# Optimization experiments

Hardware: AMD Instinct MI355X
Metric: run time of the kernel (lower is better)

## Reference

```python
import jax, jax.numpy as jnp
import numpy as np
import math

HIDDEN, N_HEADS = 128, 4
HEAD_DIM = HIDDEN // N_HEADS

def _silu(x):
    return x * jax.nn.sigmoid(x)

def _ln(x, g, b, eps=1e-5):
    m = jnp.mean(x, axis=-1, keepdims=True)
    v = jnp.mean((x - m) ** 2, axis=-1, keepdims=True)
    return (x - m) / jnp.sqrt(v + eps) * g + b


def setup_inputs() -> dict:
    key = jax.random.key(0)
    B, N, ND, ED, HD = 2, 512, 64, 32, 128
    ks = iter(jax.random.split(key, 64))
    def p(*shape):
        return jax.random.normal(next(ks), shape, jnp.float32) * 0.05
    d = {}
    d['h'] = jax.random.normal(next(ks), (B, N, ND), jnp.float32)
    d['x'] = jax.random.normal(next(ks), (B, N, 2), jnp.float32)
    d['e'] = jax.random.normal(next(ks), (B, N, N, ED), jnp.float32)
    msg_in = 2 * ND + ED + 1  # 161
    d['msg_W1'] = p(msg_in, HD); d['msg_b1'] = jnp.zeros((HD,), jnp.float32)
    d['msg_ln_g'] = jnp.ones((HD,), jnp.float32); d['msg_ln_b'] = jnp.zeros((HD,), jnp.float32)
    d['msg_W2'] = p(HD, HD); d['msg_b2'] = jnp.zeros((HD,), jnp.float32)
    d['msg_W3'] = p(HD, HD); d['msg_b3'] = jnp.zeros((HD,), jnp.float32)
    d['attn_W1'] = p(HD, HD // 2); d['attn_b1'] = jnp.zeros((HD // 2,), jnp.float32)
    d['attn_W2'] = p(HD // 2, N_HEADS); d['attn_b2'] = jnp.zeros((N_HEADS,), jnp.float32)
    d['val_W'] = p(HD, HD); d['val_b'] = jnp.zeros((HD,), jnp.float32)
    d['coord_W1'] = p(HD, HD // 2); d['coord_b1'] = jnp.zeros((HD // 2,), jnp.float32)
    d['coord_W2'] = p(HD // 2, 1)  # bias=False
    d['node_W1'] = p(ND + HD, HD); d['node_b1'] = jnp.zeros((HD,), jnp.float32)
    d['node_ln_g'] = jnp.ones((HD,), jnp.float32); d['node_ln_b'] = jnp.zeros((HD,), jnp.float32)
    d['node_W2'] = p(HD, ND); d['node_b2'] = jnp.zeros((ND,), jnp.float32)
    d['edge_W1'] = p(ED + HD, HD); d['edge_b1'] = jnp.zeros((HD,), jnp.float32)
    d['edge_ln_g'] = jnp.ones((HD,), jnp.float32); d['edge_ln_b'] = jnp.zeros((HD,), jnp.float32)
    d['edge_W2'] = p(HD, ED); d['edge_b2'] = jnp.zeros((ED,), jnp.float32)
    d['nn_g'] = jnp.ones((ND,), jnp.float32); d['nn_b'] = jnp.zeros((ND,), jnp.float32)
    d['en_g'] = jnp.ones((ED,), jnp.float32); d['en_b'] = jnp.zeros((ED,), jnp.float32)
    d['coord_scale'] = jnp.float32(0.1)
    return d


def reference(h, x, e,
              msg_W1, msg_b1, msg_ln_g, msg_ln_b, msg_W2, msg_b2, msg_W3, msg_b3,
              attn_W1, attn_b1, attn_W2, attn_b2, val_W, val_b,
              coord_W1, coord_b1, coord_W2,
              node_W1, node_b1, node_ln_g, node_ln_b, node_W2, node_b2,
              edge_W1, edge_b1, edge_ln_g, edge_ln_b, edge_W2, edge_b2,
              nn_g, nn_b, en_g, en_b, coord_scale):
    B, N, ND = h.shape
    # pairwise geometry: x_diff[b,i,j] = x[b,j] - x[b,i]
    x_diff = x[:, None, :, :] - x[:, :, None, :]           # (B,N,N,2)
    distances = jnp.linalg.norm(x_diff, axis=-1, keepdims=True)  # (B,N,N,1)
    h_i = jnp.broadcast_to(h[:, :, None, :], (B, N, N, ND))
    h_j = jnp.broadcast_to(h[:, None, :, :], (B, N, N, ND))
    msg_input = jnp.concatenate([h_i, h_j, e, distances], axis=-1)
    # message MLP (dropout is identity in eval)
    m = _silu(msg_input @ msg_W1 + msg_b1)
    m = _ln(m, msg_ln_g, msg_ln_b)
    m = _silu(m @ msg_W2 + msg_b2)
    messages = m @ msg_W3 + msg_b3                          # (B,N,N,HIDDEN)
    # attention over j (axis=2), multi-head
    attn_logits = (_silu(messages @ attn_W1 + attn_b1) @ attn_W2 + attn_b2)
    attn_logits = attn_logits / math.sqrt(HEAD_DIM)
    attn_weights = jax.nn.softmax(attn_logits, axis=2)      # (B,N,N,H)
    values = (messages @ val_W + val_b).reshape(B, N, N, N_HEADS, HEAD_DIM)
    messages_attended = jnp.einsum('bijh,bijhd->bihd', attn_weights, values)
    messages_attended = messages_attended.reshape(B, N, HIDDEN)
    # equivariant coordinate update
    coord_weights = _silu(messages @ coord_W1 + coord_b1) @ coord_W2  # (B,N,N,1)
    coord_weights = jnp.tanh(coord_weights / 10.0)
    x_diff_norm = x_diff / (distances + 1e-8)
    coord_update = jnp.sum(coord_weights * x_diff_norm, axis=2)      # (B,N,2)
    x_new = x + coord_scale * coord_update
    # node update
    h_input = jnp.concatenate([h, messages_attended], axis=-1)
    hh = _silu(h_input @ node_W1 + node_b1)
    hh = _ln(hh, node_ln_g, node_ln_b)
    hh = hh @ node_W2 + node_b2
    h_new = _ln(h + hh, nn_g, nn_b)
    # edge update
    e_input = jnp.concatenate([e, messages], axis=-1)
    ee = _silu(e_input @ edge_W1 + edge_b1)
    ee = _ln(ee, edge_ln_g, edge_ln_b)
    ee = ee @ edge_W2 + edge_b2
    e_new = _ln(e + ee, en_g, en_b)
    return (h_new, x_new, e_new)
```

## Files before the change

kernel.cpp:

```cpp
#include <hip/hip_runtime.h>
#include <math.h>

typedef __attribute__((ext_vector_type(8))) short short8;
typedef __attribute__((ext_vector_type(4))) short short4v;
typedef __attribute__((ext_vector_type(8))) unsigned short u16x8;
typedef __attribute__((ext_vector_type(4))) float f32x4;

#define NN 512
#define JT 32
#define STR 136
#define BUFSZ (JT * STR)
#define E2S 36

#define TOT_W 106496

__device__ __forceinline__ unsigned short f2b(float x) {
    unsigned int u = __float_as_uint(x);
    unsigned int r = (u + 0x7FFFu + ((u >> 16) & 1u)) >> 16;
    return (unsigned short)r;
}
__device__ __forceinline__ float b2f(unsigned short v) {
    return __uint_as_float(((unsigned int)v) << 16);
}
__device__ __forceinline__ float silu_f(float v) { return v / (1.f + __expf(-v)); }

__device__ __forceinline__ float half_sum(float v, float* s_red, int t) {
    s_red[t] = v;
    __syncthreads();
    int tt = t & 127;
    for (int s = 64; s > 0; s >>= 1) {
        if (tt < s) s_red[t] += s_red[t + s];
        __syncthreads();
    }
    float r = s_red[t & 128];
    __syncthreads();
    return r;
}

__device__ __forceinline__ void frag_kf(int loc, int nK, int& k, int& f) {
    int jj = loc & 7;
    int lane = (loc >> 3) & 63;
    int fs = loc >> 9;
    int ks = fs % nK;
    int ft = fs / nK;
    k = ks * 32 + ((lane >> 4) << 3) + jj;
    f = ft * 16 + (lane & 15);
}

extern "C" __global__ void prepack_w(const float* __restrict__ msg_W1, const float* __restrict__ msg_W2,
                                     const float* __restrict__ msg_W3, const float* __restrict__ val_W,
                                     const float* __restrict__ attn_W1, const float* __restrict__ coord_W1,
                                     const float* __restrict__ edge_W1, const float* __restrict__ edge_W2,
                                     unsigned short* __restrict__ ws) {
    int idx = blockIdx.x * 256 + threadIdx.x;
    if (idx >= TOT_W) return;
    float v;
    int k, f;
    if (idx < 16384) {
        frag_kf(idx, 4, k, f);
        v = (k <= 96) ? msg_W1[(64 + k) * 128 + f] : 0.f;
    } else if (idx < 32768) {
        frag_kf(idx - 16384, 4, k, f);
        v = msg_W2[k * 128 + f];
    } else if (idx < 49152) {
        frag_kf(idx - 32768, 4, k, f);
        v = msg_W3[k * 128 + f];
    } else if (idx < 65536) {
        frag_kf(idx - 49152, 4, k, f);
        v = val_W[k * 128 + f];
    } else if (idx < 81920) {
        frag_kf(idx - 65536, 4, k, f);
        v = (f < 64) ? attn_W1[k * 64 + f] : coord_W1[k * 64 + (f - 64)];
    } else if (idx < 102400) {
        frag_kf(idx - 81920, 5, k, f);
        v = (k < 128) ? edge_W1[(32 + k) * 128 + f] : edge_W1[(k - 128) * 128 + f];
    } else {
        frag_kf(idx - 102400, 4, k, f);
        v = edge_W2[k * 32 + f];
    }
    ws[idx] = f2b(v);
}

struct Frag2x2 { f32x4 a[2][2]; };

__device__ __forceinline__ short8 wfrag(const unsigned short* base, int nK, int ft, int ks, int lane) {
    return *(const short8*)(base + (((ft * nK + ks) << 9) + (lane << 3)));
}

__device__ __forceinline__ void initF(Frag2x2& F, const float* bias, int ftA, int lane) {
    int q = lane >> 4;
    f32x4 bA = *(const f32x4*)(bias + ftA * 16 + q * 4);
    f32x4 bB = *(const f32x4*)(bias + (ftA + 1) * 16 + q * 4);
    F.a[0][0] = bA; F.a[0][1] = bA;
    F.a[1][0] = bB; F.a[1][1] = bB;
}

__device__ __forceinline__ void ldb(const unsigned short* B, int kcol, int lane, short8& b0, short8& b1) {
    int q8 = ((lane >> 4) << 3), l15 = lane & 15;
    b0 = *(const short8*)(B + l15 * STR + kcol + q8);
    b1 = *(const short8*)(B + (16 + l15) * STR + kcol + q8);
}

__device__ __forceinline__ void mfma4(Frag2x2& F, short8 a0, short8 a1, short8 b0, short8 b1) {
    F.a[0][0] = __builtin_amdgcn_mfma_f32_16x16x32_bf16(a0, b0, F.a[0][0], 0, 0, 0);
    F.a[0][1] = __builtin_amdgcn_mfma_f32_16x16x32_bf16(a0, b1, F.a[0][1], 0, 0, 0);
    F.a[1][0] = __builtin_amdgcn_mfma_f32_16x16x32_bf16(a1, b0, F.a[1][0], 0, 0, 0);
    F.a[1][1] = __builtin_amdgcn_mfma_f32_16x16x32_bf16(a1, b1, F.a[1][1], 0, 0, 0);
}

__device__ __forceinline__ void storeF(const Frag2x2& F, unsigned short* dbuf, int ftA, int lane, int act) {
    int q = lane >> 4, l15 = lane & 15;
#pragma unroll
    for (int fi = 0; fi < 2; fi++)
#pragma unroll
        for (int ji = 0; ji < 2; ji++) {
            int j = ji * 16 + l15;
            int f0 = (ftA + fi) * 16 + q * 4;
            f32x4 v = F.a[fi][ji];
            short4v p;
#pragma unroll
            for (int r = 0; r < 4; r++) {
                float o = act ? silu_f(v[r]) : v[r];
                p[r] = (short)f2b(o);
            }
            *(short4v*)(dbuf + j * STR + f0) = p;
        }
}

__device__ __forceinline__ void ln_tile(unsigned short* buf, const float* g, const float* bv, int t) {
    int j = t >> 3, sub = t & 7;
    unsigned short* p = buf + j * STR + sub * 16;
    u16x8 r0 = *(u16x8*)p;
    u16x8 r1 = *(u16x8*)(p + 8);
    float v[16];
#pragma unroll
    for (int i = 0; i < 8; i++) { v[i] = b2f(r0[i]); v[8 + i] = b2f(r1[i]); }
    float sm = 0.f;
#pragma unroll
    for (int i = 0; i < 16; i++) sm += v[i];
    sm += __shfl_xor(sm, 1); sm += __shfl_xor(sm, 2); sm += __shfl_xor(sm, 4);
    float mean = sm * 0.0078125f;
    float sq = 0.f;
#pragma unroll
    for (int i = 0; i < 16; i++) { float d = v[i] - mean; sq += d * d; }
    sq += __shfl_xor(sq, 1); sq += __shfl_xor(sq, 2); sq += __shfl_xor(sq, 4);
    float rstd = rsqrtf(sq * 0.0078125f + 1e-5f);
    u16x8 o0, o1;
#pragma unroll
    for (int i = 0; i < 8; i++) {
        o0[i] = f2b((v[i] - mean) * rstd * g[sub * 16 + i] + bv[sub * 16 + i]);
        o1[i] = f2b((v[8 + i] - mean) * rstd * g[sub * 16 + 8 + i] + bv[sub * 16 + 8 + i]);
    }
    *(u16x8*)p = o0;
    *(u16x8*)(p + 8) = o1;
}

extern "C" __global__ __launch_bounds__(256, 2)
void egnn_mfma(const float* __restrict__ h, const float* __restrict__ x, const float* __restrict__ e,
               const float* __restrict__ msg_W1, const float* __restrict__ msg_b1,
               const float* __restrict__ msg_ln_g, const float* __restrict__ msg_ln_b,
               const float* __restrict__ msg_b2, const float* __restrict__ msg_b3,
               const float* __restrict__ attn_b1, const float* __restrict__ attn_W2,
               const float* __restrict__ attn_b2, const float* __restrict__ val_b,
               const float* __restrict__ coord_b1, const float* __restrict__ coord_W2,
               const float* __restrict__ node_W1, const float* __restrict__ node_b1,
               const float* __restrict__ node_ln_g, const float* __restrict__ node_ln_b,
               const float* __restrict__ node_W2, const float* __restrict__ node_b2,
               const float* __restrict__ edge_b1, const float* __restrict__ edge_ln_g,
               const float* __restrict__ edge_ln_b, const float* __restrict__ edge_b2,
               const float* __restrict__ nn_g, const float* __restrict__ nn_b,
               const float* __restrict__ en_g, const float* __restrict__ en_b,
               const float* __restrict__ coord_scale_p,
               const unsigned short* __restrict__ wpk,
               float* __restrict__ out_h, float* __restrict__ out_x, float* __restrict__ out_e) {
    const int t = threadIdx.x;
    const int wave = t >> 6, lane = t & 63;
    const int biA = blockIdx.x * 2;
    const int biB = biA + 1;
    const int b = biA >> 9;

    __shared__ __align__(16) unsigned short smA[3 * BUFSZ];
    __shared__ __align__(16) unsigned short smB[3 * BUFSZ];
    unsigned short* B0a = smA;
    unsigned short* B1a = smA + BUFSZ;
    unsigned short* B2a = smA + 2 * BUFSZ;
    unsigned short* B0b = smB;
    unsigned short* B1b = smB + BUFSZ;
    unsigned short* B2b = smB + 2 * BUFSZ;
    __shared__ __align__(16) unsigned short s_e2a[32 * E2S];
    __shared__ __align__(16) unsigned short s_e2b[32 * E2S];

    __shared__ __align__(16) float s_bias1a[128], s_bias1b[128];
    __shared__ __align__(16) float s_b2c[128], s_b3c[128], s_bv[128], s_bac[128], s_be1[128];
    __shared__ __align__(16) float s_be2[32];
    __shared__ __align__(16) float s_mg[128], s_mb[128], s_eg[128], s_eb[128];
    __shared__ __align__(16) float s_cw2[64], s_aw2[4][64], s_ab2[4], s_eng[32], s_enb[32];
    __shared__ __align__(16) float s_lg[2][JT][4];
    __shared__ __align__(16) float s_hiA[64], s_hiB[64];

    const unsigned short* wG1 = wpk;
    const unsigned short* wG2 = wpk + 16384;
    const unsigned short* wG3 = wpk + 32768;
    const unsigned short* wV  = wpk + 49152;
    const unsigned short* wAC = wpk + 65536;
    const unsigned short* wE1 = wpk + 81920;
    const unsigned short* wE2 = wpk + 102400;

    if (t < 64) s_hiA[t] = h[(size_t)biA * 64 + t];
    else if (t < 128) s_hiB[t - 64] = h[(size_t)biB * 64 + (t - 64)];
    if (t < 128) {
        s_b2c[t] = msg_b2[t]; s_b3c[t] = msg_b3[t]; s_bv[t] = val_b[t];
        s_bac[t] = (t < 64) ? attn_b1[t] : coord_b1[t - 64];
        s_be1[t] = edge_b1[t];
        s_mg[t] = msg_ln_g[t]; s_mb[t] = msg_ln_b[t];
        s_eg[t] = edge_ln_g[t]; s_eb[t] = edge_ln_b[t];
    }
    if (t < 32) { s_be2[t] = edge_b2[t]; s_eng[t] = en_g[t]; s_enb[t] = en_b[t]; }
    if (t < 64) s_cw2[t] = coord_W2[t];
    { int hh = t >> 6, k = t & 63; s_aw2[hh][k] = attn_W2[k * 4 + hh]; }
    if (t < 4) s_ab2[t] = attn_b2[t];
    __syncthreads();
    {
        int ii = t >> 7, tt = t & 127;
        const float* hi = ii ? s_hiB : s_hiA;
        float acc = msg_b1[tt];
        for (int k = 0; k < 64; k++) acc = fmaf(hi[k], msg_W1[k * 128 + tt], acc);
        (ii ? s_bias1b : s_bias1a)[tt] = acc;
    }
    const float xiA0 = x[(size_t)biA * 2 + 0];
    const float xiA1 = x[(size_t)biA * 2 + 1];
    const float xiB0 = x[(size_t)biB * 2 + 0];
    const float xiB1 = x[(size_t)biB * 2 + 1];

    float m_run = -3e38f, l_run = 0.f, acc_run = 0.f;
    float cu_x = 0.f, cu_y = 0.f, xdn_x = 0.f, xdn_y = 0.f;

    const int q8 = ((lane >> 4) << 3), l15 = lane & 15;

#pragma unroll 1
    for (int j0 = 0; j0 < NN; j0 += JT) {
        {
            int j = t >> 3, sub = t & 7;
            int jj = j0 + j;
            const float* hp = h + ((size_t)(b * NN + jj)) * 64 + sub * 8;
            float4 h0 = *(const float4*)hp;
            float4 h1 = *(const float4*)(hp + 4);
            u16x8 o;
            o[0] = f2b(h0.x); o[1] = f2b(h0.y); o[2] = f2b(h0.z); o[3] = f2b(h0.w);
            o[4] = f2b(h1.x); o[5] = f2b(h1.y); o[6] = f2b(h1.z); o[7] = f2b(h1.w);
            *(u16x8*)(B0a + j * STR + sub * 8) = o;
            if (sub < 4) {
                const float* ea = e + ((size_t)biA * NN + jj) * 32 + sub * 8;
                float4 e0 = *(const float4*)ea;
                float4 e1 = *(const float4*)(ea + 4);
                u16x8 oe;
                oe[0] = f2b(e0.x); oe[1] = f2b(e0.y); oe[2] = f2b(e0.z); oe[3] = f2b(e0.w);
                oe[4] = f2b(e1.x); oe[5] = f2b(e1.y); oe[6] = f2b(e1.z); oe[7] = f2b(e1.w);
                *(u16x8*)(B0a + j * STR + 64 + sub * 8) = oe;
                const float* eb = e + ((size_t)biB * NN + jj) * 32 + sub * 8;
                float4 f0v = *(const float4*)eb;
                float4 f1v = *(const float4*)(eb + 4);
                u16x8 ob;
                ob[0] = f2b(f0v.x); ob[1] = f2b(f0v.y); ob[2] = f2b(f0v.z); ob[3] = f2b(f0v.w);
                ob[4] = f2b(f1v.x); ob[5] = f2b(f1v.y); ob[6] = f2b(f1v.z); ob[7] = f2b(f1v.w);
                *(u16x8*)(B0b + j * STR + 64 + sub * 8) = ob;
            } else if (sub > 4) {
                u16x8 z = (u16x8)0;
                *(u16x8*)(B0a + j * STR + 96 + (sub - 4) * 8) = z;
                *(u16x8*)(B0b + j * STR + 96 + (sub - 4) * 8) = z;
            }
        }
        if (t < JT) {
            int jj = j0 + t;
            float dx = x[(size_t)(b * NN + jj) * 2 + 0] - xiA0;
            float dy = x[(size_t)(b * NN + jj) * 2 + 1] - xiA1;
            float dist = sqrtf(dx * dx + dy * dy);
            float inv = 1.f / (dist + 1e-8f);
            xdn_x = dx * inv; xdn_y = dy * inv;
            u16x8 z = (u16x8)0;
            z[0] = f2b(dist);
            *(u16x8*)(B0a + t * STR + 96) = z;
        } else if (t >= 128 && t < 128 + JT) {
            int tb = t - 128;
            int jj = j0 + tb;
            float dx = x[(size_t)(b * NN + jj) * 2 + 0] - xiB0;
            float dy = x[(size_t)(b * NN + jj) * 2 + 1] - xiB1;
            float dist = sqrtf(dx * dx + dy * dy);
            float inv = 1.f / (dist + 1e-8f);
            xdn_x = dx * inv; xdn_y = dy * inv;
            u16x8 z = (u16x8)0;
            z[0] = f2b(dist);
            *(u16x8*)(B0b + tb * STR + 96) = z;
        }
        __syncthreads();

        {
            Frag2x2 Fa, Fb;
            initF(Fa, s_bias1a, wave * 2, lane);
            initF(Fb, s_bias1b, wave * 2, lane);
#pragma unroll
            for (int ks = 0; ks < 4; ks++) {
                short8 a0 = wfrag(wG1, 4, wave * 2, ks, lane);
                short8 a1 = wfrag(wG1, 4, wave * 2 + 1, ks, lane);
                short8 b0, b1;
                ldb(B0a, ks * 32, lane, b0, b1);
                mfma4(Fa, a0, a1, b0, b1);
                if (ks >= 2) ldb(B0b, ks * 32, lane, b0, b1);
                mfma4(Fb, a0, a1, b0, b1);
            }
            storeF(Fa, B1a, wave * 2, lane, 1);
            storeF(Fb, B1b, wave * 2, lane, 1);
        }
        __syncthreads();
        ln_tile(B1a, s_mg, s_mb, t);
        ln_tile(B1b, s_mg, s_mb, t);
        __syncthreads();

        {
            Frag2x2 Fa, Fb;
            initF(Fa, s_b2c, wave * 2, lane);
            initF(Fb, s_b2c, wave * 2, lane);
#pragma unroll
            for (int ks = 0; ks < 4; ks++) {
                short8 a0 = wfrag(wG2, 4, wave * 2, ks, lane);
                short8 a1 = wfrag(wG2, 4, wave * 2 + 1, ks, lane);
                short8 b0, b1;
                ldb(B1a, ks * 32, lane, b0, b1); mfma4(Fa, a0, a1, b0, b1);
                ldb(B1b, ks * 32, lane, b0, b1); mfma4(Fb, a0, a1, b0, b1);
            }
            storeF(Fa, B2a, wave * 2, lane, 1);
            storeF(Fb, B2b, wave * 2, lane, 1);
        }
        __syncthreads();

        {
            Frag2x2 Fa, Fb;
            initF(Fa, s_b3c, wave * 2, lane);
            initF(Fb, s_b3c, wave * 2, lane);
#pragma unroll
            for (int ks = 0; ks < 4; ks++) {
                short8 a0 = wfrag(wG3, 4, wave * 2, ks, lane);
                short8 a1 = wfrag(wG3, 4, wave * 2 + 1, ks, lane);
                short8 b0, b1;
                ldb(B2a, ks * 32, lane, b0, b1); mfma4(Fa, a0, a1, b0, b1);
                ldb(B2b, ks * 32, lane, b0, b1); mfma4(Fb, a0, a1, b0, b1);
            }
            storeF(Fa, B1a, wave * 2, lane, 0);
            storeF(Fb, B1b, wave * 2, lane, 0);
        }
        __syncthreads();

        {
            Frag2x2 FEa, FEb;
            initF(FEa, s_be1, wave * 2, lane);
            initF(FEb, s_be1, wave * 2, lane);
            {
                short8 a0 = wfrag(wE1, 5, wave * 2, 4, lane);
                short8 a1 = wfrag(wE1, 5, wave * 2 + 1, 4, lane);
                short8 b0, b1;
                ldb(B0a, 64, lane, b0, b1); mfma4(FEa, a0, a1, b0, b1);
                ldb(B0b, 64, lane, b0, b1); mfma4(FEb, a0, a1, b0, b1);
            }
            Frag2x2 FVa, FVb, FAa, FAb;
            initF(FVa, s_bv, wave * 2, lane);
            initF(FVb, s_bv, wave * 2, lane);
            initF(FAa, s_bac, wave * 2, lane);
            initF(FAb, s_bac, wave * 2, lane);
#pragma unroll
            for (int ks = 0; ks < 4; ks++) {
                short8 av0 = wfrag(wV, 4, wave * 2, ks, lane);
                short8 av1 = wfrag(wV, 4, wave * 2 + 1, ks, lane);
                short8 aa0 = wfrag(wAC, 4, wave * 2, ks, lane);
                short8 aa1 = wfrag(wAC, 4, wave * 2 + 1, ks, lane);
                short8 b0, b1;
                ldb(B1a, ks * 32, lane, b0, b1);
                mfma4(FVa, av0, av1, b0, b1);
                mfma4(FAa, aa0, aa1, b0, b1);
                ldb(B1b, ks * 32, lane, b0, b1);
                mfma4(FVb, av0, av1, b0, b1);
                mfma4(FAb, aa0, aa1, b0, b1);
            }
            storeF(FVa, B2a, wave * 2, lane, 0);
            storeF(FVb, B2b, wave * 2, lane, 0);
#pragma unroll
            for (int ks = 0; ks < 4; ks++) {
                short8 ae0 = wfrag(wE1, 5, wave * 2, ks, lane);
                short8 ae1 = wfrag(wE1, 5, wave * 2 + 1, ks, lane);
                short8 b0, b1;
                ldb(B1a, ks * 32, lane, b0, b1); mfma4(FEa, ae0, ae1, b0, b1);
                ldb(B1b, ks * 32, lane, b0, b1); mfma4(FEb, ae0, ae1, b0, b1);
            }
            __syncthreads();
            storeF(FAa, B0a, wave * 2, lane, 1);
            storeF(FAb, B0b, wave * 2, lane, 1);
            storeF(FEa, B1a, wave * 2, lane, 1);
            storeF(FEb, B1b, wave * 2, lane, 1);
        }
        __syncthreads();

        ln_tile(B1a, s_eg, s_eb, t);
        ln_tile(B1b, s_eg, s_eb, t);
        {
            int ii = t >> 7, tt = t & 127;
            const unsigned short* B0x = ii ? B0b : B0a;
            int j = tt >> 2, hh = tt & 3;
            float acc = s_ab2[hh];
#pragma unroll
            for (int m = 0; m < 8; m++) {
                u16x8 r = *(u16x8*)(B0x + j * STR + m * 8);
#pragma unroll
                for (int i = 0; i < 8; i++) acc = fmaf(b2f(r[i]), s_aw2[hh][m * 8 + i], acc);
            }
            s_lg[ii][j][hh] = acc * 0.17677669529663687f;
        }
        __syncthreads();

        {
            int ii = t >> 7, tt = t & 127;
            const unsigned short* B2x = ii ? B2b : B2a;
            int hh = tt >> 5;
#pragma unroll 4
            for (int j = 0; j < JT; j++) {
                float lg = s_lg[ii][j][hh];
                float nm = fmaxf(m_run, lg);
                float sc = __expf(m_run - nm);
                float p = __expf(lg - nm);
                float v = b2f(B2x[j * STR + tt]);
                acc_run = acc_run * sc + p * v;
                l_run = l_run * sc + p;
                m_run = nm;
            }
            if (tt < 32) {
                const unsigned short* B0x = ii ? B0b : B0a;
                float acc = 0.f;
#pragma unroll
                for (int m = 0; m < 8; m++) {
                    u16x8 r = *(u16x8*)(B0x + tt * STR + 64 + m * 8);
#pragma unroll
                    for (int i = 0; i < 8; i++) acc = fmaf(b2f(r[i]), s_cw2[m * 8 + i], acc);
                }
                float cw = tanhf(acc * 0.1f);
                cu_x = fmaf(cw, xdn_x, cu_x);
                cu_y = fmaf(cw, xdn_y, cu_y);
            }
        }
        __syncthreads();

        {
            int ih = wave >> 1, wv = wave & 1;
            const unsigned short* B1x = ih ? B1b : B1a;
            unsigned short* e2x = ih ? s_e2b : s_e2a;
            int q = lane >> 4;
            f32x4 bb = *(const f32x4*)(s_be2 + wv * 16 + q * 4);
            f32x4 a0 = bb, a1 = bb;
#pragma unroll
            for (int ks = 0; ks < 4; ks++) {
                short8 b0, b1;
                ldb(B1x, ks * 32, lane, b0, b1);
                short8 aw = wfrag(wE2, 4, wv, ks, lane);
                a0 = __builtin_amdgcn_mfma_f32_16x16x32_bf16(aw, b0, a0, 0, 0, 0);
                a1 = __builtin_amdgcn_mfma_f32_16x16x32_bf16(aw, b1, a1, 0, 0, 0);
            }
#pragma unroll
            for (int ji = 0; ji < 2; ji++) {
                int j = ji * 16 + l15;
                int f0 = wv * 16 + q * 4;
                f32x4 v = ji ? a1 : a0;
                short4v p;
#pragma unroll
                for (int r = 0; r < 4; r++) p[r] = (short)f2b(v[r]);
                *(short4v*)(e2x + j * E2S + f0) = p;
            }
        }
        __syncthreads();

#pragma unroll
        for (int ii = 0; ii < 2; ii++) {
            int biX = biA + ii;
            const unsigned short* e2x = ii ? s_e2b : s_e2a;
            int j = t >> 3, sub = t & 7;
            int jj = j0 + j;
            float4 ev = *(const float4*)(e + ((size_t)biX * NN + jj) * 32 + sub * 4);
            const unsigned short* p = e2x + j * E2S + sub * 4;
            float v0 = ev.x + b2f(p[0]);
            float v1 = ev.y + b2f(p[1]);
            float v2 = ev.z + b2f(p[2]);
            float v3 = ev.w + b2f(p[3]);
            float s = v0 + v1 + v2 + v3;
            s += __shfl_xor(s, 1); s += __shfl_xor(s, 2); s += __shfl_xor(s, 4);
            float mean = s * 0.03125f;
            float d0 = v0 - mean, d1 = v1 - mean, d2 = v2 - mean, d3 = v3 - mean;
            float sq = d0 * d0 + d1 * d1 + d2 * d2 + d3 * d3;
            sq += __shfl_xor(sq, 1); sq += __shfl_xor(sq, 2); sq += __shfl_xor(sq, 4);
            float rstd = rsqrtf(sq * 0.03125f + 1e-5f);
            float4 o;
            o.x = d0 * rstd * s_eng[sub * 4 + 0] + s_enb[sub * 4 + 0];
            o.y = d1 * rstd * s_eng[sub * 4 + 1] + s_enb[sub * 4 + 1];
            o.z = d2 * rstd * s_eng[sub * 4 + 2] + s_enb[sub * 4 + 2];
            o.w = d3 * rstd * s_eng[sub * 4 + 3] + s_enb[sub * 4 + 3];
            *(float4*)(out_e + ((size_t)biX * NN + jj) * 32 + sub * 4) = o;
        }
    }

    float* s_ep = (float*)smA;
    float* s_hinA = s_ep;
    float* s_hinB = s_ep + 192;
    float* s_nhA  = s_ep + 384;
    float* s_nhB  = s_ep + 512;
    float* s_red  = s_ep + 640;

    __syncthreads();
    {
        int ii = t >> 7, tt = t & 127;
        (ii ? s_hinB : s_hinA)[64 + tt] = acc_run / l_run;
    }
    if (t < 64) s_hinA[t] = s_hiA[t];
    else if (t < 128) s_hinB[t - 64] = s_hiB[t - 64];
    __syncthreads();

    {
        int ii = t >> 7, tt = t & 127;
        const float* hin = ii ? s_hinB : s_hinA;
        float acc = node_b1[tt];
        for (int k4 = 0; k4 < 48; k4++) {
            float4 iv = *(const float4*)&hin[k4 * 4];
            acc = fmaf(iv.x, node_W1[(k4 * 4 + 0) * 128 + tt], acc);
            acc = fmaf(iv.y, node_W1[(k4 * 4 + 1) * 128 + tt], acc);
            acc = fmaf(iv.z, node_W1[(k4 * 4 + 2) * 128 + tt], acc);
            acc = fmaf(iv.w, node_W1[(k4 * 4 + 3) * 128 + tt], acc);
        }
        (ii ? s_nhB : s_nhA)[tt] = silu_f(acc);
    }
    __syncthreads();
    {
        int ii = t >> 7, tt = t & 127;
        float* nh = ii ? s_nhB : s_nhA;
        float v = nh[tt];
        float mean = half_sum(v, s_red, t) * 0.0078125f;
        float d = v - mean;
        float var = half_sum(d * d, s_red, t) * 0.0078125f;
        float rstd = rsqrtf(var + 1e-5f);
        nh[tt] = d * rstd * node_ln_g[tt] + node_ln_b[tt];
    }
    __syncthreads();
    {
        int ii = t >> 7, tt = t & 127;
        float hv = 0.f;
        if (tt < 64) {
            const float* nh = ii ? s_nhB : s_nhA;
            float acc = node_b2[tt];
            for (int k4 = 0; k4 < 32; k4++) {
                float4 iv = *(const float4*)&nh[k4 * 4];
                acc = fmaf(iv.x, node_W2[(k4 * 4 + 0) * 64 + tt], acc);
                acc = fmaf(iv.y, node_W2[(k4 * 4 + 1) * 64 + tt], acc);
                acc = fmaf(iv.z, node_W2[(k4 * 4 + 2) * 64 + tt], acc);
                acc = fmaf(iv.w, node_W2[(k4 * 4 + 3) * 64 + tt], acc);
            }
            hv = acc + (ii ? s_hiB : s_hiA)[tt];
        }
        float mean = half_sum((tt < 64) ? hv : 0.f, s_red, t) * 0.015625f;
        float d = (tt < 64) ? (hv - mean) : 0.f;
        float var = half_sum(d * d, s_red, t) * 0.015625f;
        float rstd = rsqrtf(var + 1e-5f);
        if (tt < 64) out_h[(size_t)(biA + ii) * 64 + tt] = d * rstd * nn_g[tt] + nn_b[tt];
    }

    {
        int tt = t & 127;
        if (tt < 32) {
            cu_x += __shfl_xor(cu_x, 16); cu_x += __shfl_xor(cu_x, 8);
            cu_x += __shfl_xor(cu_x, 4);  cu_x += __shfl_xor(cu_x, 2); cu_x += __shfl_xor(cu_x, 1);
            cu_y += __shfl_xor(cu_y, 16); cu_y += __shfl_xor(cu_y, 8);
            cu_y += __shfl_xor(cu_y, 4);  cu_y += __shfl_xor(cu_y, 2); cu_y += __shfl_xor(cu_y, 1);
            if (tt == 0) {
                float scl = coord_scale_p[0];
                if (t < 32) {
                    out_x[(size_t)biA * 2 + 0] = xiA0 + scl * cu_x;
                    out_x[(size_t)biA * 2 + 1] = xiA1 + scl * cu_y;
                } else {
                    out_x[(size_t)biB * 2 + 0] = xiB0 + scl * cu_x;
                    out_x[(size_t)biB * 2 + 1] = xiB1 + scl * cu_y;
                }
            }
        }
    }
}

extern "C" void kernel_launch(void* const* d_in, const int* in_sizes, int n_in,
                              void* d_out, int out_size, void* d_ws, size_t ws_size,
                              hipStream_t stream) {
    const float* h        = (const float*)d_in[0];
    const float* x        = (const float*)d_in[1];
    const float* e        = (const float*)d_in[2];
    const float* msg_W1   = (const float*)d_in[3];
    const float* msg_b1   = (const float*)d_in[4];
    const float* msg_ln_g = (const float*)d_in[5];
    const float* msg_ln_b = (const float*)d_in[6];
    const float* msg_W2   = (const float*)d_in[7];
    const float* msg_b2   = (const float*)d_in[8];
    const float* msg_W3   = (const float*)d_in[9];
    const float* msg_b3   = (const float*)d_in[10];
    const float* attn_W1  = (const float*)d_in[11];
    const float* attn_b1  = (const float*)d_in[12];
    const float* attn_W2  = (const float*)d_in[13];
    const float* attn_b2  = (const float*)d_in[14];
    const float* val_W    = (const float*)d_in[15];
    const float* val_b    = (const float*)d_in[16];
    const float* coord_W1 = (const float*)d_in[17];
    const float* coord_b1 = (const float*)d_in[18];
    const float* coord_W2 = (const float*)d_in[19];
    const float* node_W1  = (const float*)d_in[20];
    const float* node_b1  = (const float*)d_in[21];
    const float* node_ln_g= (const float*)d_in[22];
    const float* node_ln_b= (const float*)d_in[23];
    const float* node_W2  = (const float*)d_in[24];
    const float* node_b2  = (const float*)d_in[25];
    const float* edge_W1  = (const float*)d_in[26];
    const float* edge_b1  = (const float*)d_in[27];
    const float* edge_ln_g= (const float*)d_in[28];
    const float* edge_ln_b= (const float*)d_in[29];
    const float* edge_W2  = (const float*)d_in[30];
    const float* edge_b2  = (const float*)d_in[31];
    const float* nn_g     = (const float*)d_in[32];
    const float* nn_b     = (const float*)d_in[33];
    const float* en_g     = (const float*)d_in[34];
    const float* en_b     = (const float*)d_in[35];
    const float* coord_scale = (const float*)d_in[36];

    unsigned short* wpk = (unsigned short*)d_ws;

    float* out = (float*)d_out;
    float* out_h = out;
    float* out_x = out + (size_t)2 * 512 * 64;
    float* out_e = out_x + (size_t)2 * 512 * 2;

    hipLaunchKernelGGL(prepack_w, dim3((TOT_W + 255) / 256), dim3(256), 0, stream,
                       msg_W1, msg_W2, msg_W3, val_W, attn_W1, coord_W1, edge_W1, edge_W2, wpk);

    hipLaunchKernelGGL(egnn_mfma, dim3(512), dim3(256), 0, stream,
                       h, x, e,
                       msg_W1, msg_b1, msg_ln_g, msg_ln_b, msg_b2, msg_b3,
                       attn_b1, attn_W2, attn_b2, val_b, coord_b1, coord_W2,
                       node_W1, node_b1, node_ln_g, node_ln_b, node_W2, node_b2,
                       edge_b1, edge_ln_g, edge_ln_b, edge_b2,
                       nn_g, nn_b, en_g, en_b, coord_scale,
                       wpk, out_h, out_x, out_e);
}
```

Baseline: 719.9 us.

## Double block to 512 threads, one feature tile per wave, overlap attention and edge stages

Raises the block from 256 to 512 threads (8 waves), so each wave computes one 16-wide output feature tile instead of two. This halves per-wave accumulator registers and raises the number of waves per block. The attention/value/coord stage (waves 0-3) now runs concurrently with the edge-W2 stage (waves 4-7), removing one barrier. The edge-W1 MFMAs are fused into the value/attn loop, and the e tile load is hoisted before the barrier. The risks are reduced MFMA reuse of each B fragment across waves and the occupancy limit set by launch_bounds(512,4).

```diff
diff --git a/kernel.cpp b/kernel.cpp
--- a/kernel.cpp
+++ b/kernel.cpp
@@ -24,15 +24,15 @@
 }
 __device__ __forceinline__ float silu_f(float v) { return v / (1.f + __expf(-v)); }
 
-__device__ __forceinline__ float half_sum(float v, float* s_red, int t) {
-    s_red[t] = v;
+__device__ __forceinline__ float half_sum512(float v, float* s_red, int t) {
+    if (t < 256) s_red[t] = v;
     __syncthreads();
     int tt = t & 127;
     for (int s = 64; s > 0; s >>= 1) {
-        if (tt < s) s_red[t] += s_red[t + s];
-        __syncthreads();
-    }
-    float r = s_red[t & 128];
+        if (t < 256 && tt < s) s_red[t] += s_red[t + s];
+        __syncthreads();
+    }
+    float r = (t < 256) ? s_red[t & 128] : 0.f;
     __syncthreads();
     return r;
 }
@@ -81,18 +81,16 @@
     ws[idx] = f2b(v);
 }
 
-struct Frag2x2 { f32x4 a[2][2]; };
+struct Frag1 { f32x4 a[2]; };
 
 __device__ __forceinline__ short8 wfrag(const unsigned short* base, int nK, int ft, int ks, int lane) {
     return *(const short8*)(base + (((ft * nK + ks) << 9) + (lane << 3)));
 }
 
-__device__ __forceinline__ void initF(Frag2x2& F, const float* bias, int ftA, int lane) {
+__device__ __forceinline__ void initF1(Frag1& F, const float* bias, int ft, int lane) {
     int q = lane >> 4;
-    f32x4 bA = *(const f32x4*)(bias + ftA * 16 + q * 4);
-    f32x4 bB = *(const f32x4*)(bias + (ftA + 1) * 16 + q * 4);
-    F.a[0][0] = bA; F.a[0][1] = bA;
-    F.a[1][0] = bB; F.a[1][1] = bB;
+    f32x4 bv = *(const f32x4*)(bias + ft * 16 + q * 4);
+    F.a[0] = bv; F.a[1] = bv;
 }
 
 __device__ __forceinline__ void ldb(const unsigned short* B, int kcol, int lane, short8& b0, short8& b1) {
@@ -101,34 +99,30 @@
     b1 = *(const short8*)(B + (16 + l15) * STR + kcol + q8);
 }
 
-__device__ __forceinline__ void mfma4(Frag2x2& F, short8 a0, short8 a1, short8 b0, short8 b1) {
-    F.a[0][0] = __builtin_amdgcn_mfma_f32_16x16x32_bf16(a0, b0, F.a[0][0], 0, 0, 0);
-    F.a[0][1] = __builtin_amdgcn_mfma_f32_16x16x32_bf16(a0, b1, F.a[0][1], 0, 0, 0);
-    F.a[1][0] = __builtin_amdgcn_mfma_f32_16x16x32_bf16(a1, b0, F.a[1][0], 0, 0, 0);
-    F.a[1][1] = __builtin_amdgcn_mfma_f32_16x16x32_bf16(a1, b1, F.a[1][1], 0, 0, 0);
-}
-
-__device__ __forceinline__ void storeF(const Frag2x2& F, unsigned short* dbuf, int ftA, int lane, int act) {
+__device__ __forceinline__ void mfma2(Frag1& F, short8 a, short8 b0, short8 b1) {
+    F.a[0] = __builtin_amdgcn_mfma_f32_16x16x32_bf16(a, b0, F.a[0], 0, 0, 0);
+    F.a[1] = __builtin_amdgcn_mfma_f32_16x16x32_bf16(a, b1, F.a[1], 0, 0, 0);
+}
+
+__device__ __forceinline__ void storeF1(const Frag1& F, unsigned short* dbuf, int ft, int lane, int act) {
     int q = lane >> 4, l15 = lane & 15;
 #pragma unroll
-    for (int fi = 0; fi < 2; fi++)
-#pragma unroll
-        for (int ji = 0; ji < 2; ji++) {
-            int j = ji * 16 + l15;
-            int f0 = (ftA + fi) * 16 + q * 4;
-            f32x4 v = F.a[fi][ji];
-            short4v p;
-#pragma unroll
-            for (int r = 0; r < 4; r++) {
-                float o = act ? silu_f(v[r]) : v[r];
-                p[r] = (short)f2b(o);
-            }
-            *(short4v*)(dbuf + j * STR + f0) = p;
-        }
-}
-
-__device__ __forceinline__ void ln_tile(unsigned short* buf, const float* g, const float* bv, int t) {
-    int j = t >> 3, sub = t & 7;
+    for (int ji = 0; ji < 2; ji++) {
+        int j = ji * 16 + l15;
+        int f0 = ft * 16 + q * 4;
+        f32x4 v = F.a[ji];
+        short4v p;
+#pragma unroll
+        for (int r = 0; r < 4; r++) {
+            float o = act ? silu_f(v[r]) : v[r];
+            p[r] = (short)f2b(o);
+        }
+        *(short4v*)(dbuf + j * STR + f0) = p;
+    }
+}
+
+__device__ __forceinline__ void ln_tile(unsigned short* buf, const float* g, const float* bv, int tt) {
+    int j = tt >> 3, sub = tt & 7;
     unsigned short* p = buf + j * STR + sub * 16;
     u16x8 r0 = *(u16x8*)p;
     u16x8 r1 = *(u16x8*)(p + 8);
@@ -155,7 +149,7 @@
     *(u16x8*)(p + 8) = o1;
 }
 
-extern "C" __global__ __launch_bounds__(256, 2)
+extern "C" __global__ __launch_bounds__(512, 4)
 void egnn_mfma(const float* __restrict__ h, const float* __restrict__ x, const float* __restrict__ e,
                const float* __restrict__ msg_W1, const float* __restrict__ msg_b1,
                const float* __restrict__ msg_ln_g, const float* __restrict__ msg_ln_b,
@@ -217,10 +211,10 @@
     }
     if (t < 32) { s_be2[t] = edge_b2[t]; s_eng[t] = en_g[t]; s_enb[t] = en_b[t]; }
     if (t < 64) s_cw2[t] = coord_W2[t];
-    { int hh = t >> 6, k = t & 63; s_aw2[hh][k] = attn_W2[k * 4 + hh]; }
+    if (t < 256) { int hh = t >> 6, k = t & 63; s_aw2[hh][k] = attn_W2[k * 4 + hh]; }
     if (t < 4) s_ab2[t] = attn_b2[t];
     __syncthreads();
-    {
+    if (t < 256) {
         int ii = t >> 7, tt = t & 127;
         const float* hi = ii ? s_hiB : s_hiA;
         float acc = msg_b1[tt];
@@ -235,39 +229,43 @@
     float m_run = -3e38f, l_run = 0.f, acc_run = 0.f;
     float cu_x = 0.f, cu_y = 0.f, xdn_x = 0.f, xdn_y = 0.f;
 
-    const int q8 = ((lane >> 4) << 3), l15 = lane & 15;
+    const int l15 = lane & 15;
 
 #pragma unroll 1
     for (int j0 = 0; j0 < NN; j0 += JT) {
         {
-            int j = t >> 3, sub = t & 7;
+            int half = t >> 8, tt = t & 255;
+            int j = tt >> 3, sub = tt & 7;
             int jj = j0 + j;
-            const float* hp = h + ((size_t)(b * NN + jj)) * 64 + sub * 8;
-            float4 h0 = *(const float4*)hp;
-            float4 h1 = *(const float4*)(hp + 4);
-            u16x8 o;
-            o[0] = f2b(h0.x); o[1] = f2b(h0.y); o[2] = f2b(h0.z); o[3] = f2b(h0.w);
-            o[4] = f2b(h1.x); o[5] = f2b(h1.y); o[6] = f2b(h1.z); o[7] = f2b(h1.w);
-            *(u16x8*)(B0a + j * STR + sub * 8) = o;
-            if (sub < 4) {
-                const float* ea = e + ((size_t)biA * NN + jj) * 32 + sub * 8;
-                float4 e0 = *(const float4*)ea;
-                float4 e1 = *(const float4*)(ea + 4);
-                u16x8 oe;
-                oe[0] = f2b(e0.x); oe[1] = f2b(e0.y); oe[2] = f2b(e0.z); oe[3] = f2b(e0.w);
-                oe[4] = f2b(e1.x); oe[5] = f2b(e1.y); oe[6] = f2b(e1.z); oe[7] = f2b(e1.w);
-                *(u16x8*)(B0a + j * STR + 64 + sub * 8) = oe;
-                const float* eb = e + ((size_t)biB * NN + jj) * 32 + sub * 8;
-                float4 f0v = *(const float4*)eb;
-                float4 f1v = *(const float4*)(eb + 4);
-                u16x8 ob;
-                ob[0] = f2b(f0v.x); ob[1] = f2b(f0v.y); ob[2] = f2b(f0v.z); ob[3] = f2b(f0v.w);
-                ob[4] = f2b(f1v.x); ob[5] = f2b(f1v.y); ob[6] = f2b(f1v.z); ob[7] = f2b(f1v.w);
-                *(u16x8*)(B0b + j * STR + 64 + sub * 8) = ob;
-            } else if (sub > 4) {
+            if (half == 0) {
+                const float* hp = h + ((size_t)(b * NN + jj)) * 64 + sub * 8;
+                float4 h0 = *(const float4*)hp;
+                float4 h1 = *(const float4*)(hp + 4);
+                u16x8 o;
+                o[0] = f2b(h0.x); o[1] = f2b(h0.y); o[2] = f2b(h0.z); o[3] = f2b(h0.w);
+                o[4] = f2b(h1.x); o[5] = f2b(h1.y); o[6] = f2b(h1.z); o[7] = f2b(h1.w);
+                *(u16x8*)(B0a + j * STR + sub * 8) = o;
                 u16x8 z = (u16x8)0;
-                *(u16x8*)(B0a + j * STR + 96 + (sub - 4) * 8) = z;
-                *(u16x8*)(B0b + j * STR + 96 + (sub - 4) * 8) = z;
+                if (sub > 4)       *(u16x8*)(B0a + j * STR + 96 + (sub - 4) * 8) = z;
+                else if (sub >= 1) *(u16x8*)(B0b + j * STR + 96 + sub * 8) = z;
+            } else {
+                if (sub < 4) {
+                    const float* ea = e + ((size_t)biA * NN + jj) * 32 + sub * 8;
+                    float4 e0 = *(const float4*)ea;
+                    float4 e1 = *(const float4*)(ea + 4);
+                    u16x8 oe;
+                    oe[0] = f2b(e0.x); oe[1] = f2b(e0.y); oe[2] = f2b(e0.z); oe[3] = f2b(e0.w);
+                    oe[4] = f2b(e1.x); oe[5] = f2b(e1.y); oe[6] = f2b(e1.z); oe[7] = f2b(e1.w);
+                    *(u16x8*)(B0a + j * STR + 64 + sub * 8) = oe;
+                } else {
+                    const float* eb = e + ((size_t)biB * NN + jj) * 32 + (sub - 4) * 8;
+                    float4 e0 = *(const float4*)eb;
+                    float4 e1 = *(const float4*)(eb + 4);
+                    u16x8 oe;
+                    oe[0] = f2b(e0.x); oe[1] = f2b(e0.y); oe[2] = f2b(e0.z); oe[3] = f2b(e0.w);
+                    oe[4] = f2b(e1.x); oe[5] = f2b(e1.y); oe[6] = f2b(e1.z); oe[7] = f2b(e1.w);
+                    *(u16x8*)(B0b + j * STR + 64 + (sub - 4) * 8) = oe;
+                }
             }
         }
         if (t < JT) {
@@ -295,127 +293,118 @@
         __syncthreads();
 
         {
-            Frag2x2 Fa, Fb;
-            initF(Fa, s_bias1a, wave * 2, lane);
-            initF(Fb, s_bias1b, wave * 2, lane);
+            Frag1 Fa, Fb;
+            initF1(Fa, s_bias1a, wave, lane);
+            initF1(Fb, s_bias1b, wave, lane);
 #pragma unroll
             for (int ks = 0; ks < 4; ks++) {
-                short8 a0 = wfrag(wG1, 4, wave * 2, ks, lane);
-                short8 a1 = wfrag(wG1, 4, wave * 2 + 1, ks, lane);
+                short8 a = wfrag(wG1, 4, wave, ks, lane);
                 short8 b0, b1;
                 ldb(B0a, ks * 32, lane, b0, b1);
-                mfma4(Fa, a0, a1, b0, b1);
+                mfma2(Fa, a, b0, b1);
                 if (ks >= 2) ldb(B0b, ks * 32, lane, b0, b1);
-                mfma4(Fb, a0, a1, b0, b1);
-            }
-            storeF(Fa, B1a, wave * 2, lane, 1);
-            storeF(Fb, B1b, wave * 2, lane, 1);
-        }
-        __syncthreads();
-        ln_tile(B1a, s_mg, s_mb, t);
-        ln_tile(B1b, s_mg, s_mb, t);
+                mfma2(Fb, a, b0, b1);
+            }
+            storeF1(Fa, B1a, wave, lane, 1);
+            storeF1(Fb, B1b, wave, lane, 1);
+        }
+        __syncthreads();
+        if (t < 256) ln_tile(B1a, s_mg, s_mb, t);
+        else         ln_tile(B1b, s_mg, s_mb, t - 256);
         __syncthreads();
 
         {
-            Frag2x2 Fa, Fb;
-            initF(Fa, s_b2c, wave * 2, lane);
-            initF(Fb, s_b2c, wave * 2, lane);
+            Frag1 Fa, Fb;
+            initF1(Fa, s_b2c, wave, lane);
+            initF1(Fb, s_b2c, wave, lane);
 #pragma unroll
             for (int ks = 0; ks < 4; ks++) {
-                short8 a0 = wfrag(wG2, 4, wave * 2, ks, lane);
-                short8 a1 = wfrag(wG2, 4, wave * 2 + 1, ks, lane);
+                short8 a = wfrag(wG2, 4, wave, ks, lane);
                 short8 b0, b1;
-                ldb(B1a, ks * 32, lane, b0, b1); mfma4(Fa, a0, a1, b0, b1);
-                ldb(B1b, ks * 32, lane, b0, b1); mfma4(Fb, a0, a1, b0, b1);
-            }
-            storeF(Fa, B2a, wave * 2, lane, 1);
-            storeF(Fb, B2b, wave * 2, lane, 1);
+                ldb(B1a, ks * 32, lane, b0, b1); mfma2(Fa, a, b0, b1);
+                ldb(B1b, ks * 32, lane, b0, b1); mfma2(Fb, a, b0, b1);
+            }
+            storeF1(Fa, B2a, wave, lane, 1);
+            storeF1(Fb, B2b, wave, lane, 1);
         }
         __syncthreads();
 
         {
-            Frag2x2 Fa, Fb;
-            initF(Fa, s_b3c, wave * 2, lane);
-            initF(Fb, s_b3c, wave * 2, lane);
+            Frag1 Fa, Fb;
+            initF1(Fa, s_b3c, wave, lane);
+            initF1(Fb, s_b3c, wave, lane);
 #pragma unroll
             for (int ks = 0; ks < 4; ks++) {
-                short8 a0 = wfrag(wG3, 4, wave * 2, ks, lane);
-                short8 a1 = wfrag(wG3, 4, wave * 2 + 1, ks, lane);
+                short8 a = wfrag(wG3, 4, wave, ks, lane);
                 short8 b0, b1;
-                ldb(B2a, ks * 32, lane, b0, b1); mfma4(Fa, a0, a1, b0, b1);
-                ldb(B2b, ks * 32, lane, b0, b1); mfma4(Fb, a0, a1, b0, b1);
-            }
-            storeF(Fa, B1a, wave * 2, lane, 0);
-            storeF(Fb, B1b, wave * 2, lane, 0);
+                ldb(B2a, ks * 32, lane, b0, b1); mfma2(Fa, a, b0, b1);
+                ldb(B2b, ks * 32, lane, b0, b1); mfma2(Fb, a, b0, b1);
+            }
+            storeF1(Fa, B1a, wave, lane, 0);
+            storeF1(Fb, B1b, wave, lane, 0);
         }
         __syncthreads();
 
         {
-            Frag2x2 FEa, FEb;
-            initF(FEa, s_be1, wave * 2, lane);
-            initF(FEb, s_be1, wave * 2, lane);
+            Frag1 FEa, FEb;
+            initF1(FEa, s_be1, wave, lane);
+            initF1(FEb, s_be1, wave, lane);
             {
-                short8 a0 = wfrag(wE1, 5, wave * 2, 4, lane);
-                short8 a1 = wfrag(wE1, 5, wave * 2 + 1, 4, lane);
+                short8 a = wfrag(wE1, 5, wave, 4, lane);
                 short8 b0, b1;
-                ldb(B0a, 64, lane, b0, b1); mfma4(FEa, a0, a1, b0, b1);
-                ldb(B0b, 64, lane, b0, b1); mfma4(FEb, a0, a1, b0, b1);
-            }
-            Frag2x2 FVa, FVb, FAa, FAb;
-            initF(FVa, s_bv, wave * 2, lane);
-            initF(FVb, s_bv, wave * 2, lane);
-            initF(FAa, s_bac, wave * 2, lane);
-            initF(FAb, s_bac, wave * 2, lane);
+                ldb(B0a, 64, lane, b0, b1); mfma2(FEa, a, b0, b1);
+                ldb(B0b, 64, lane, b0, b1); mfma2(FEb, a, b0, b1);
+            }
+            Frag1 FVa, FVb, FAa, FAb;
+            initF1(FVa, s_bv, wave, lane);
+            initF1(FVb, s_bv, wave, lane);
+            initF1(FAa, s_bac, wave, lane);
+            initF1(FAb, s_bac, wave, lane);
 #pragma unroll
             for (int ks = 0; ks < 4; ks++) {
-                short8 av0 = wfrag(wV, 4, wave * 2, ks, lane);
-                short8 av1 = wfrag(wV, 4, wave * 2 + 1, ks, lane);
-                short8 aa0 = wfrag(wAC, 4, wave * 2, ks, lane);
-                short8 aa1 = wfrag(wAC, 4, wave * 2 + 1, ks, lane);
+                short8 av = wfrag(wV, 4, wave, ks, lane);
+                short8 aa = wfrag(wAC, 4, wave, ks, lane);
+                short8 ae = wfrag(wE1, 5, wave, ks, lane);
                 short8 b0, b1;
                 ldb(B1a, ks * 32, lane, b0, b1);
-                mfma4(FVa, av0, av1, b0, b1);
-                mfma4(FAa, aa0, aa1, b0, b1);
+                mfma2(FVa, av, b0, b1); mfma2(FAa, aa, b0, b1); mfma2(FEa, ae, b0, b1);
                 ldb(B1b, ks * 32, lane, b0, b1);
-                mfma4(FVb, av0, av1, b0, b1);
-                mfma4(FAb, aa0, aa1, b0, b1);
-            }
-            storeF(FVa, B2a, wave * 2, lane, 0);
-            storeF(FVb, B2b, wave * 2, lane, 0);
-#pragma unroll
-            for (int ks = 0; ks < 4; ks++) {
-                short8 ae0 = wfrag(wE1, 5, wave * 2, ks, lane);
-                short8 ae1 = wfrag(wE1, 5, wave * 2 + 1, ks, lane);
-                short8 b0, b1;
-                ldb(B1a, ks * 32, lane, b0, b1); mfma4(FEa, ae0, ae1, b0, b1);
-                ldb(B1b, ks * 32, lane, b0, b1); mfma4(FEb, ae0, ae1, b0, b1);
-            }
+                mfma2(FVb, av, b0, b1); mfma2(FAb, aa, b0, b1); mfma2(FEb, ae, b0, b1);
+            }
+            storeF1(FVa, B2a, wave, lane, 0);
+            storeF1(FVb, B2b, wave, lane, 0);
             __syncthreads();
-            storeF(FAa, B0a, wave * 2, lane, 1);
-            storeF(FAb, B0b, wave * 2, lane, 1);
-            storeF(FEa, B1a, wave * 2, lane, 1);
-            storeF(FEb, B1b, wave * 2, lane, 1);
-        }
-        __syncthreads();
-
-        ln_tile(B1a, s_eg, s_eb, t);
-        ln_tile(B1b, s_eg, s_eb, t);
-        {
-            int ii = t >> 7, tt = t & 127;
+            storeF1(FAa, B0a, wave, lane, 1);
+            storeF1(FAb, B0b, wave, lane, 1);
+            storeF1(FEa, B1a, wave, lane, 1);
+            storeF1(FEb, B1b, wave, lane, 1);
+        }
+        __syncthreads();
+
+        if (t < 256) {
+            ln_tile(B1a, s_eg, s_eb, t);
+        } else {
+            ln_tile(B1b, s_eg, s_eb, t - 256);
+            int m = t - 256;
+            int ii = m >> 7, mm = m & 127;
             const unsigned short* B0x = ii ? B0b : B0a;
-            int j = tt >> 2, hh = tt & 3;
+            int j = mm >> 2, hh = mm & 3;
             float acc = s_ab2[hh];
 #pragma unroll
-            for (int m = 0; m < 8; m++) {
-                u16x8 r = *(u16x8*)(B0x + j * STR + m * 8);
-#pragma unroll
-                for (int i = 0; i < 8; i++) acc = fmaf(b2f(r[i]), s_aw2[hh][m * 8 + i], acc);
+            for (int m8 = 0; m8 < 8; m8++) {
+                u16x8 r = *(u16x8*)(B0x + j * STR + m8 * 8);
+#pragma unroll
+                for (int i = 0; i < 8; i++) acc = fmaf(b2f(r[i]), s_aw2[hh][m8 * 8 + i], acc);
             }
             s_lg[ii][j][hh] = acc * 0.17677669529663687f;
         }
         __syncthreads();
 
-        {
+        const int ii9 = t >> 8, tt9 = t & 255;
+        const int j9 = tt9 >> 3, sub9 = tt9 & 7;
+        float4 ev = *(const float4*)(e + ((size_t)(biA + ii9) * NN + (j0 + j9)) * 32 + sub9 * 4);
+
+        if (wave < 4) {
             int ii = t >> 7, tt = t & 127;
             const unsigned short* B2x = ii ? B2b : B2a;
             int hh = tt >> 5;
@@ -443,11 +432,8 @@
                 cu_x = fmaf(cw, xdn_x, cu_x);
                 cu_y = fmaf(cw, xdn_y, cu_y);
             }
-        }
-        __syncthreads();
-
-        {
-            int ih = wave >> 1, wv = wave & 1;
+        } else {
+            int w4 = wave - 4, ih = w4 >> 1, wv = w4 & 1;
             const unsigned short* B1x = ih ? B1b : B1a;
             unsigned short* e2x = ih ? s_e2b : s_e2a;
             int q = lane >> 4;
@@ -474,14 +460,9 @@
         }
         __syncthreads();
 
-#pragma unroll
-        for (int ii = 0; ii < 2; ii++) {
-            int biX = biA + ii;
-            const unsigned short* e2x = ii ? s_e2b : s_e2a;
-            int j = t >> 3, sub = t & 7;
-            int jj = j0 + j;
-            float4 ev = *(const float4*)(e + ((size_t)biX * NN + jj) * 32 + sub * 4);
-            const unsigned short* p = e2x + j * E2S + sub * 4;
+        {
+            const unsigned short* e2x = ii9 ? s_e2b : s_e2a;
+            const unsigned short* p = e2x + j9 * E2S + sub9 * 4;
             float v0 = ev.x + b2f(p[0]);
             float v1 = ev.y + b2f(p[1]);
             float v2 = ev.z + b2f(p[2]);
@@ -494,11 +475,11 @@
             sq += __shfl_xor(sq, 1); sq += __shfl_xor(sq, 2); sq += __shfl_xor(sq, 4);
             float rstd = rsqrtf(sq * 0.03125f + 1e-5f);
             float4 o;
-            o.x = d0 * rstd * s_eng[sub * 4 + 0] + s_enb[sub * 4 + 0];
-            o.y = d1 * rstd * s_eng[sub * 4 + 1] + s_enb[sub * 4 + 1];
-            o.z = d2 * rstd * s_eng[sub * 4 + 2] + s_enb[sub * 4 + 2];
-            o.w = d3 * rstd * s_eng[sub * 4 + 3] + s_enb[sub * 4 + 3];
-            *(float4*)(out_e + ((size_t)biX * NN + jj) * 32 + sub * 4) = o;
+            o.x = d0 * rstd * s_eng[sub9 * 4 + 0] + s_enb[sub9 * 4 + 0];
+            o.y = d1 * rstd * s_eng[sub9 * 4 + 1] + s_enb[sub9 * 4 + 1];
+            o.z = d2 * rstd * s_eng[sub9 * 4 + 2] + s_enb[sub9 * 4 + 2];
+            o.w = d3 * rstd * s_eng[sub9 * 4 + 3] + s_enb[sub9 * 4 + 3];
+            *(float4*)(out_e + ((size_t)(biA + ii9) * NN + (j0 + j9)) * 32 + sub9 * 4) = o;
         }
     }
 
@@ -510,7 +491,7 @@
     float* s_red  = s_ep + 640;
 
     __syncthreads();
-    {
+    if (t < 256) {
         int ii = t >> 7, tt = t & 127;
         (ii ? s_hinB : s_hinA)[64 + tt] = acc_run / l_run;
     }
@@ -518,7 +499,7 @@
     else if (t < 128) s_hinB[t - 64] = s_hiB[t - 64];
     __syncthreads();
 
-    {
+    if (t < 256) {
         int ii = t >> 7, tt = t & 127;
         const float* hin = ii ? s_hinB : s_hinA;
         float acc = node_b1[tt];
@@ -534,19 +515,18 @@
     __syncthreads();
     {
         int ii = t >> 7, tt = t & 127;
-        float* nh = ii ? s_nhB : s_nhA;
-        float v = nh[tt];
-        float mean = half_sum(v, s_red, t) * 0.0078125f;
-        float d = v - mean;
-        float var = half_sum(d * d, s_red, t) * 0.0078125f;
+        float v = (t < 256) ? (ii ? s_nhB : s_nhA)[tt] : 0.f;
+        float mean = half_sum512(v, s_red, t) * 0.0078125f;
+        float d = (t < 256) ? (v - mean) : 0.f;
+        float var = half_sum512(d * d, s_red, t) * 0.0078125f;
         float rstd = rsqrtf(var + 1e-5f);
-        nh[tt] = d * rstd * node_ln_g[tt] + node_ln_b[tt];
+        if (t < 256) (ii ? s_nhB : s_nhA)[tt] = d * rstd * node_ln_g[tt] + node_ln_b[tt];
     }
     __syncthreads();
     {
         int ii = t >> 7, tt = t & 127;
         float hv = 0.f;
-        if (tt < 64) {
+        if (t < 256 && tt < 64) {
             const float* nh = ii ? s_nhB : s_nhA;
             float acc = node_b2[tt];
             for (int k4 = 0; k4 < 32; k4++) {
@@ -558,14 +538,14 @@
             }
             hv = acc + (ii ? s_hiB : s_hiA)[tt];
         }
-        float mean = half_sum((tt < 64) ? hv : 0.f, s_red, t) * 0.015625f;
-        float d = (tt < 64) ? (hv - mean) : 0.f;
-        float var = half_sum(d * d, s_red, t) * 0.015625f;
+        float mean = half_sum512((t < 256 && tt < 64) ? hv : 0.f, s_red, t) * 0.015625f;
+        float d = (t < 256 && tt < 64) ? (hv - mean) : 0.f;
+        float var = half_sum512(d * d, s_red, t) * 0.015625f;
         float rstd = rsqrtf(var + 1e-5f);
-        if (tt < 64) out_h[(size_t)(biA + ii) * 64 + tt] = d * rstd * nn_g[tt] + nn_b[tt];
-    }
-
-    {
+        if (t < 256 && tt < 64) out_h[(size_t)(biA + ii) * 64 + tt] = d * rstd * nn_g[tt] + nn_b[tt];
+    }
+
+    if (t < 256) {
         int tt = t & 127;
         if (tt < 32) {
             cu_x += __shfl_xor(cu_x, 16); cu_x += __shfl_xor(cu_x, 8);
@@ -637,7 +617,7 @@
     hipLaunchKernelGGL(prepack_w, dim3((TOT_W + 255) / 256), dim3(256), 0, stream,
                        msg_W1, msg_W2, msg_W3, val_W, attn_W1, coord_W1, edge_W1, edge_W2, wpk);
 
-    hipLaunchKernelGGL(egnn_mfma, dim3(512), dim3(256), 0, stream,
+    hipLaunchKernelGGL(egnn_mfma, dim3(512), dim3(512), 0, stream,
                        h, x, e,
                        msg_W1, msg_b1, msg_ln_g, msg_ln_b, msg_b2, msg_b3,
                        attn_b1, attn_W2, attn_b2, val_b, coord_b1, coord_W2,
```

Result: faster. 649.2 us (-9.8%).
